# Kernel tuning notes

Measured on AMD Instinct MI355X. Metric: run time of the kernel, lower is better.

Reference implementation:

```python
import jax, jax.numpy as jnp
import numpy as np

B, S, IN_DIM = 2, 2048, 1024
DIMS, QH, KVH = 1024, 16, 4
HD = DIMS // QH          # head_dims = 64
G = QH // KVH            # groups = 4


def setup_inputs() -> dict:
    key = jax.random.key(0)
    k1, k2, k3, k4, k5, k6 = jax.random.split(key, 6)
    scale = 0.02
    q_in = jax.random.normal(k1, (B, S, IN_DIM), dtype=jnp.float32)
    kv_in = jax.random.normal(k2, (B, S, IN_DIM), dtype=jnp.float32)
    # causal mask (True = attend)
    mask = jnp.tril(jnp.ones((S, S), dtype=bool))
    Wq = jax.random.normal(k3, (IN_DIM, QH, HD), dtype=jnp.float32) * scale
    Wk = jax.random.normal(k4, (IN_DIM, KVH, HD), dtype=jnp.float32) * scale
    Wv = jax.random.normal(k5, (IN_DIM, KVH, HD), dtype=jnp.float32) * scale
    Wo = jax.random.normal(k6, (KVH * HD, IN_DIM), dtype=jnp.float32) * scale
    return {"q_in": q_in, "kv_in": kv_in, "mask": mask,
            "Wq": Wq, "Wk": Wk, "Wv": Wv, "Wo": Wo}


def reference(q_in, kv_in, mask, Wq, Wk, Wv, Wo):
    b, s, _ = q_in.shape
    # projections (DenseGeneral, no bias)
    q = jnp.einsum('bsi,ihd->bshd', q_in, Wq)   # [B,S,QH,HD]
    k = jnp.einsum('bsi,ihd->bshd', kv_in, Wk)  # [B,S,KVH,HD]
    v = jnp.einsum('bsi,ihd->bshd', kv_in, Wv)  # [B,S,KVH,HD]
    # rearrange '... s (h g) d -> ... g h s d' with g=G (h outer, g inner),
    # then einsum '... g h s d, ... h a d -> ... h s a' sums over g.
    # Equivalent (and cheaper): sum q over the group axis first.
    q_g = q.reshape(b, s, KVH, G, HD).sum(axis=3)        # [B,S,KVH,HD]
    q_g = jnp.transpose(q_g, (0, 2, 1, 3))               # [B,KVH,S,HD]
    k = jnp.transpose(k, (0, 2, 1, 3))                   # [B,KVH,S,HD]
    v = jnp.transpose(v, (0, 2, 1, 3))                   # [B,KVH,S,HD]
    scores = jnp.einsum('bhsd,bhad->bhsa', q_g, k)       # [B,KVH,S,S]
    scores = jnp.where(mask[None, None, :, :], scores, -jnp.inf)
    attn = jax.nn.softmax(scores / (HD ** 0.5), axis=-1)
    out = jnp.einsum('bhsa,bhad->bhsd', attn, v)         # [B,KVH,S,HD]
    out = jnp.transpose(out, (0, 2, 1, 3)).reshape(b, s, KVH * HD)
    return out @ Wo                                      # [B,S,IN_DIM]
```

## Files before the change

kernel.cpp:

```cpp
#include <hip/hip_runtime.h>
#include <hip/hip_bf16.h>

#define SS 2048
#define NSPLIT 8

typedef __attribute__((ext_vector_type(8))) short bf16x8;
typedef __attribute__((ext_vector_type(4))) float f32x4;

__device__ __forceinline__ short f2bf(float f){
    unsigned u = __float_as_uint(f);
    u += 0x7fff + ((u >> 16) & 1);
    return (short)(u >> 16);
}
__device__ __forceinline__ float bf2f(short s){
    return __uint_as_float(((unsigned)(unsigned short)s) << 16);
}

__global__ __launch_bounds__(256) void k_prep_w(const float* __restrict__ Wq,
                                                const float* __restrict__ Wk,
                                                const float* __restrict__ Wv,
                                                const float* __restrict__ Wo,
                                                short* __restrict__ WcatT,
                                                short* __restrict__ WoT){
    __shared__ float Ts[64][65];
    const int bx = blockIdx.x;
    const int r  = threadIdx.x >> 2;
    const int cq = (threadIdx.x & 3) * 16;
    if (bx < 192) {
        const int ktile = bx & 15, ntile = bx >> 4;
        const int k0 = ktile * 64, n0 = ntile * 64;
        if (ntile < 4) {
            const float* base = Wq + (size_t)(k0 + r) * 1024 + ntile * 256;
            #pragma unroll
            for (int i = 0; i < 16; i += 4) {
                float4 a = *(const float4*)(base + cq + i);
                float4 b = *(const float4*)(base + 64 + cq + i);
                float4 c = *(const float4*)(base + 128 + cq + i);
                float4 d = *(const float4*)(base + 192 + cq + i);
                Ts[r][cq+i]   = 0.125f * (a.x + b.x + c.x + d.x);
                Ts[r][cq+i+1] = 0.125f * (a.y + b.y + c.y + d.y);
                Ts[r][cq+i+2] = 0.125f * (a.z + b.z + c.z + d.z);
                Ts[r][cq+i+3] = 0.125f * (a.w + b.w + c.w + d.w);
            }
        } else {
            const float* W = (ntile < 8) ? Wk : Wv;
            const float* base = W + (size_t)(k0 + r) * 256 + (ntile & 3) * 64;
            #pragma unroll
            for (int i = 0; i < 16; i += 4) {
                float4 a = *(const float4*)(base + cq + i);
                Ts[r][cq+i] = a.x; Ts[r][cq+i+1] = a.y;
                Ts[r][cq+i+2] = a.z; Ts[r][cq+i+3] = a.w;
            }
        }
        __syncthreads();
        short tmp[16];
        #pragma unroll
        for (int i = 0; i < 16; ++i) tmp[i] = f2bf(Ts[cq+i][r]);
        short* dst = WcatT + (size_t)(n0 + r) * 1024 + k0 + cq;
        *(bf16x8*)dst       = *(bf16x8*)&tmp[0];
        *(bf16x8*)(dst + 8) = *(bf16x8*)&tmp[8];
    } else {
        const int b2 = bx - 192;
        const int ktile = b2 & 3, ntile = b2 >> 2;
        const int k0 = ktile * 64, n0 = ntile * 64;
        const float* base = Wo + (size_t)(k0 + r) * 1024 + n0;
        #pragma unroll
        for (int i = 0; i < 16; i += 4) {
            float4 a = *(const float4*)(base + cq + i);
            Ts[r][cq+i] = a.x; Ts[r][cq+i+1] = a.y;
            Ts[r][cq+i+2] = a.z; Ts[r][cq+i+3] = a.w;
        }
        __syncthreads();
        short tmp[16];
        #pragma unroll
        for (int i = 0; i < 16; ++i) tmp[i] = f2bf(Ts[cq+i][r]);
        short* dst = WoT + (size_t)(n0 + r) * 256 + k0 + cq;
        *(bf16x8*)dst       = *(bf16x8*)&tmp[0];
        *(bf16x8*)(dst + 8) = *(bf16x8*)&tmp[8];
    }
}

#define AS(r, c) SMEM[(r) * 72 + (c)]
#define BS(r, c) SMEM[128 * 72 + (r) * 72 + (c)]
__global__ __launch_bounds__(256) void k_gemm1(const float* __restrict__ q_in,
                                               const float* __restrict__ kv_in,
                                               const short* __restrict__ WcatT,
                                               short* __restrict__ pqk,
                                               short* __restrict__ vt){
    const int m0 = blockIdx.x * 128;
    const int n0 = blockIdx.y * 128;
    const float* X = (n0 < 256) ? q_in : kv_in;
    const int tid = threadIdx.x;
    const int wave = tid >> 6, lane = tid & 63, quad = lane >> 4, l16 = lane & 15;
    const int wrow = (wave & 1) * 64, wcol = (wave >> 1) * 64;
    const int r = tid >> 2, cc = (tid & 3) * 16;

    __shared__ short SMEM[2 * 128 * 72];

    f32x4 acc[4][4];
    #pragma unroll
    for (int tm = 0; tm < 4; ++tm)
        #pragma unroll
        for (int tn = 0; tn < 4; ++tn) acc[tm][tn] = f32x4{0.f,0.f,0.f,0.f};

    short ta0[16], ta1[16];
    bf16x8 rb0, rb1, rb2, rb3;
    {
        const float* a0 = X + (size_t)(m0 + r) * 1024 + cc;
        const float* a1 = a0 + (size_t)64 * 1024;
        #pragma unroll
        for (int i = 0; i < 16; i += 4) {
            float4 f = *(const float4*)(a0 + i);
            ta0[i] = f2bf(f.x); ta0[i+1] = f2bf(f.y); ta0[i+2] = f2bf(f.z); ta0[i+3] = f2bf(f.w);
            float4 g = *(const float4*)(a1 + i);
            ta1[i] = f2bf(g.x); ta1[i+1] = f2bf(g.y); ta1[i+2] = f2bf(g.z); ta1[i+3] = f2bf(g.w);
        }
        const short* b0 = WcatT + (size_t)(n0 + r) * 1024 + cc;
        const short* b1 = b0 + (size_t)64 * 1024;
        rb0 = *(const bf16x8*)b0; rb1 = *(const bf16x8*)(b0 + 8);
        rb2 = *(const bf16x8*)b1; rb3 = *(const bf16x8*)(b1 + 8);
    }

    for (int k0 = 0; k0 < 1024; k0 += 64) {
        *(bf16x8*)&AS(r, cc)          = *(bf16x8*)&ta0[0];
        *(bf16x8*)&AS(r, cc + 8)      = *(bf16x8*)&ta0[8];
        *(bf16x8*)&AS(r + 64, cc)     = *(bf16x8*)&ta1[0];
        *(bf16x8*)&AS(r + 64, cc + 8) = *(bf16x8*)&ta1[8];
        *(bf16x8*)&BS(r, cc)          = rb0;
        *(bf16x8*)&BS(r, cc + 8)      = rb1;
        *(bf16x8*)&BS(r + 64, cc)     = rb2;
        *(bf16x8*)&BS(r + 64, cc + 8) = rb3;
        __syncthreads();
        if (k0 + 64 < 1024) {
            const float* a0 = X + (size_t)(m0 + r) * 1024 + k0 + 64 + cc;
            const float* a1 = a0 + (size_t)64 * 1024;
            #pragma unroll
            for (int i = 0; i < 16; i += 4) {
                float4 f = *(const float4*)(a0 + i);
                ta0[i] = f2bf(f.x); ta0[i+1] = f2bf(f.y); ta0[i+2] = f2bf(f.z); ta0[i+3] = f2bf(f.w);
                float4 g = *(const float4*)(a1 + i);
                ta1[i] = f2bf(g.x); ta1[i+1] = f2bf(g.y); ta1[i+2] = f2bf(g.z); ta1[i+3] = f2bf(g.w);
            }
            const short* b0 = WcatT + (size_t)(n0 + r) * 1024 + k0 + 64 + cc;
            const short* b1 = b0 + (size_t)64 * 1024;
            rb0 = *(const bf16x8*)b0; rb1 = *(const bf16x8*)(b0 + 8);
            rb2 = *(const bf16x8*)b1; rb3 = *(const bf16x8*)(b1 + 8);
        }
        #pragma unroll
        for (int ks = 0; ks < 2; ++ks) {
            bf16x8 a[4];
            #pragma unroll
            for (int tm = 0; tm < 4; ++tm)
                a[tm] = *(bf16x8*)&AS(wrow + tm * 16 + l16, ks * 32 + quad * 8);
            #pragma unroll
            for (int tn = 0; tn < 4; ++tn) {
                bf16x8 b = *(bf16x8*)&BS(wcol + tn * 16 + l16, ks * 32 + quad * 8);
                #pragma unroll
                for (int tm = 0; tm < 4; ++tm)
                    acc[tm][tn] = __builtin_amdgcn_mfma_f32_16x16x32_bf16(a[tm], b, acc[tm][tn], 0, 0, 0);
            }
        }
        __syncthreads();
    }
    if (n0 < 512) {
        #pragma unroll
        for (int tm = 0; tm < 4; ++tm) {
            const int mrow = m0 + wrow + tm * 16 + quad * 4;
            #pragma unroll
            for (int tn = 0; tn < 4; ++tn) {
                const int col = n0 + wcol + tn * 16 + l16;
                #pragma unroll
                for (int rg = 0; rg < 4; ++rg)
                    pqk[(size_t)(mrow + rg) * 512 + col] = f2bf(acc[tm][tn][rg]);
            }
        }
    } else {
        #pragma unroll
        for (int tm = 0; tm < 4; ++tm) {
            const int ml = wrow + tm * 16 + quad * 4;
            #pragma unroll
            for (int tn = 0; tn < 4; ++tn) {
                const int cl = wcol + tn * 16 + l16;
                #pragma unroll
                for (int rg = 0; rg < 4; ++rg)
                    SMEM[cl * 136 + ml + rg] = f2bf(acc[tm][tn][rg]);
            }
        }
        __syncthreads();
        const int row  = tid >> 1;
        const int half = tid & 1;
        const int colv = (n0 - 512) + row;
        const int vh = colv >> 6, d = colv & 63;
        const int batch = m0 >> 11;
        const int s0 = (m0 & 2047) + half * 64;
        short* dst = vt + ((size_t)((batch * 4 + vh) * 64 + d)) * 2048 + s0;
        const short* src = &SMEM[row * 136 + half * 64];
        #pragma unroll
        for (int i = 0; i < 64; i += 8)
            *(bf16x8*)(dst + i) = *(const bf16x8*)(src + i);
    }
}

__global__ __launch_bounds__(256) void k_attn4(const short* __restrict__ pqk,
                                               const short* __restrict__ vt,
                                               short* __restrict__ Op,
                                               float* __restrict__ Lp){
    const int bx = blockIdx.x;
    const int qt = 31 - (bx / NSPLIT);
    const int s  = bx - (bx / NSPLIT) * NSPLIT;
    const int kv = blockIdx.y, batch = blockIdx.z;
    const int tid = threadIdx.x;
    const int wave = tid >> 6, lane = tid & 63, quad = lane >> 4, l16 = lane & 15;
    const int r = tid >> 2, c = (tid & 3) * 16;
    const int part = (((batch * 4 + kv) * 32 + qt) * NSPLIT + s);

    __shared__ short Ks[64][72];
    __shared__ short Vs[64][72];
    __shared__ short Ps[64][72];

    const size_t qrow = (size_t)(batch * SS + qt * 64 + wave * 16 + l16);
    bf16x8 aq0 = *(const bf16x8*)(pqk + qrow * 512 + kv * 64 + quad * 8);
    bf16x8 aq1 = *(const bf16x8*)(pqk + qrow * 512 + kv * 64 + 32 + quad * 8);

    f32x4 accO[4];
    #pragma unroll
    for (int t = 0; t < 4; ++t) accO[t] = f32x4{0.f, 0.f, 0.f, 0.f};
    float lrow[4] = {0.f, 0.f, 0.f, 0.f};

    bf16x8 rk0, rk1, rv0, rv1;
    int kt = s;
    if (kt <= qt) {
        const short* ksrc = pqk + (size_t)(batch * SS + kt * 64 + r) * 512 + 256 + kv * 64 + c;
        rk0 = *(const bf16x8*)ksrc; rk1 = *(const bf16x8*)(ksrc + 8);
        const short* vsrc = vt + ((size_t)((batch * 4 + kv) * 64 + r)) * 2048 + kt * 64 + c;
        rv0 = *(const bf16x8*)vsrc; rv1 = *(const bf16x8*)(vsrc + 8);
    }
    for (; kt <= qt; kt += NSPLIT) {
        *(bf16x8*)&Ks[r][c]     = rk0;
        *(bf16x8*)&Ks[r][c + 8] = rk1;
        *(bf16x8*)&Vs[r][c]     = rv0;
        *(bf16x8*)&Vs[r][c + 8] = rv1;
        __syncthreads();
        if (kt + NSPLIT <= qt) {
            const short* ksrc = pqk + (size_t)(batch * SS + (kt + NSPLIT) * 64 + r) * 512 + 256 + kv * 64 + c;
            rk0 = *(const bf16x8*)ksrc; rk1 = *(const bf16x8*)(ksrc + 8);
            const short* vsrc = vt + ((size_t)((batch * 4 + kv) * 64 + r)) * 2048 + (kt + NSPLIT) * 64 + c;
            rv0 = *(const bf16x8*)vsrc; rv1 = *(const bf16x8*)(vsrc + 8);
        }

        f32x4 sc[4];
        #pragma unroll
        for (int t = 0; t < 4; ++t) sc[t] = f32x4{0.f, 0.f, 0.f, 0.f};
        #pragma unroll
        for (int ks = 0; ks < 2; ++ks) {
            bf16x8 a = ks ? aq1 : aq0;
            #pragma unroll
            for (int t = 0; t < 4; ++t) {
                bf16x8 b = *(bf16x8*)&Ks[t * 16 + l16][ks * 32 + quad * 8];
                sc[t] = __builtin_amdgcn_mfma_f32_16x16x32_bf16(a, b, sc[t], 0, 0, 0);
            }
        }
        if (kt == qt) {
            #pragma unroll
            for (int t = 0; t < 4; ++t) {
                int colg = t * 16 + l16;
                #pragma unroll
                for (int rg = 0; rg < 4; ++rg)
                    if (colg > wave * 16 + quad * 4 + rg) sc[t][rg] = -1e30f;
            }
        }
        #pragma unroll
        for (int t = 0; t < 4; ++t) {
            #pragma unroll
            for (int rg = 0; rg < 4; ++rg) {
                float p = __expf(sc[t][rg]);
                lrow[rg] += p;
                Ps[wave * 16 + quad * 4 + rg][t * 16 + l16] = f2bf(p);
            }
        }
        #pragma unroll
        for (int ks = 0; ks < 2; ++ks) {
            bf16x8 ap = *(bf16x8*)&Ps[wave * 16 + l16][ks * 32 + quad * 8];
            #pragma unroll
            for (int t = 0; t < 4; ++t) {
                bf16x8 bv = *(bf16x8*)&Vs[t * 16 + l16][ks * 32 + quad * 8];
                accO[t] = __builtin_amdgcn_mfma_f32_16x16x32_bf16(ap, bv, accO[t], 0, 0, 0);
            }
        }
        __syncthreads();
    }
    #pragma unroll
    for (int rg = 0; rg < 4; ++rg) {
        float l = lrow[rg];
        l += __shfl_xor(l, 1);
        l += __shfl_xor(l, 2);
        l += __shfl_xor(l, 4);
        l += __shfl_xor(l, 8);
        lrow[rg] = l;
    }
    #pragma unroll
    for (int rg = 0; rg < 4; ++rg) {
        int row = wave * 16 + quad * 4 + rg;
        #pragma unroll
        for (int t = 0; t < 4; ++t)
            Op[(size_t)part * 4096 + row * 64 + t * 16 + l16] = f2bf(accO[t][rg]);
    }
    if (l16 == 0) {
        #pragma unroll
        for (int rg = 0; rg < 4; ++rg)
            Lp[part * 64 + (wave * 16 + quad * 4 + rg)] = lrow[rg];
    }
}

__global__ __launch_bounds__(256) void k_combine(const short* __restrict__ Op,
                                                 const float* __restrict__ Lp,
                                                 short* __restrict__ ao){
    const int qt = blockIdx.x, kv = blockIdx.y, batch = blockIdx.z;
    const int tid = threadIdx.x;
    const int rr = tid >> 2, cs = (tid & 3) * 16;
    const int pbase = ((batch * 4 + kv) * 32 + qt) * NSPLIT;
    float lsum = 0.f;
    #pragma unroll
    for (int i = 0; i < NSPLIT; ++i) lsum += Lp[(pbase + i) * 64 + rr];
    float inv = 1.f / lsum;
    float o[16];
    #pragma unroll
    for (int j = 0; j < 16; ++j) o[j] = 0.f;
    #pragma unroll
    for (int i = 0; i < NSPLIT; ++i) {
        const short* src = Op + (size_t)(pbase + i) * 4096 + rr * 64 + cs;
        bf16x8 v0 = *(const bf16x8*)src;
        bf16x8 v1 = *(const bf16x8*)(src + 8);
        #pragma unroll
        for (int j = 0; j < 8; ++j) { o[j] += bf2f(v0[j]); o[j + 8] += bf2f(v1[j]); }
    }
    short* dst = ao + (size_t)(batch * SS + qt * 64 + rr) * 256 + kv * 64 + cs;
    #pragma unroll
    for (int j = 0; j < 16; ++j)
        dst[j] = f2bf(o[j] * inv);
}

__global__ __launch_bounds__(256) void k_gemm2(const short* __restrict__ ao,
                                               const short* __restrict__ WoT,
                                               float* __restrict__ out){
    const int m0 = blockIdx.x * 128;
    const int n0 = blockIdx.y * 128;
    const int tid = threadIdx.x;
    const int wave = tid >> 6, lane = tid & 63, quad = lane >> 4, l16 = lane & 15;
    const int wrow = (wave & 1) * 64, wcol = (wave >> 1) * 64;
    const int r = tid >> 2, cc = (tid & 3) * 16;

    __shared__ short As[128][72];
    __shared__ short Bs[128][72];

    f32x4 acc[4][4];
    #pragma unroll
    for (int tm = 0; tm < 4; ++tm)
        #pragma unroll
        for (int tn = 0; tn < 4; ++tn) acc[tm][tn] = f32x4{0.f,0.f,0.f,0.f};

    bf16x8 ra0, ra1, ra2, ra3, rb0, rb1, rb2, rb3;
    {
        const short* a0 = ao + (size_t)(m0 + r) * 256 + cc;
        const short* a1 = a0 + (size_t)64 * 256;
        const short* b0 = WoT + (size_t)(n0 + r) * 256 + cc;
        const short* b1 = b0 + (size_t)64 * 256;
        ra0 = *(const bf16x8*)a0; ra1 = *(const bf16x8*)(a0 + 8);
        ra2 = *(const bf16x8*)a1; ra3 = *(const bf16x8*)(a1 + 8);
        rb0 = *(const bf16x8*)b0; rb1 = *(const bf16x8*)(b0 + 8);
        rb2 = *(const bf16x8*)b1; rb3 = *(const bf16x8*)(b1 + 8);
    }
    for (int k0 = 0; k0 < 256; k0 += 64) {
        *(bf16x8*)&As[r][cc]          = ra0;
        *(bf16x8*)&As[r][cc + 8]      = ra1;
        *(bf16x8*)&As[r + 64][cc]     = ra2;
        *(bf16x8*)&As[r + 64][cc + 8] = ra3;
        *(bf16x8*)&Bs[r][cc]          = rb0;
        *(bf16x8*)&Bs[r][cc + 8]      = rb1;
        *(bf16x8*)&Bs[r + 64][cc]     = rb2;
        *(bf16x8*)&Bs[r + 64][cc + 8] = rb3;
        __syncthreads();
        if (k0 + 64 < 256) {
            const short* a0 = ao + (size_t)(m0 + r) * 256 + k0 + 64 + cc;
            const short* a1 = a0 + (size_t)64 * 256;
            const short* b0 = WoT + (size_t)(n0 + r) * 256 + k0 + 64 + cc;
            const short* b1 = b0 + (size_t)64 * 256;
            ra0 = *(const bf16x8*)a0; ra1 = *(const bf16x8*)(a0 + 8);
            ra2 = *(const bf16x8*)a1; ra3 = *(const bf16x8*)(a1 + 8);
            rb0 = *(const bf16x8*)b0; rb1 = *(const bf16x8*)(b0 + 8);
            rb2 = *(const bf16x8*)b1; rb3 = *(const bf16x8*)(b1 + 8);
        }
        #pragma unroll
        for (int ks = 0; ks < 2; ++ks) {
            bf16x8 a[4];
            #pragma unroll
            for (int tm = 0; tm < 4; ++tm)
                a[tm] = *(bf16x8*)&As[wrow + tm * 16 + l16][ks * 32 + quad * 8];
            #pragma unroll
            for (int tn = 0; tn < 4; ++tn) {
                bf16x8 b = *(bf16x8*)&Bs[wcol + tn * 16 + l16][ks * 32 + quad * 8];
                #pragma unroll
                for (int tm = 0; tm < 4; ++tm)
                    acc[tm][tn] = __builtin_amdgcn_mfma_f32_16x16x32_bf16(a[tm], b, acc[tm][tn], 0, 0, 0);
            }
        }
        __syncthreads();
    }
    #pragma unroll
    for (int tm = 0; tm < 4; ++tm) {
        const int mrow = m0 + wrow + tm * 16 + quad * 4;
        #pragma unroll
        for (int tn = 0; tn < 4; ++tn) {
            const int col = n0 + wcol + tn * 16 + l16;
            #pragma unroll
            for (int rg = 0; rg < 4; ++rg)
                out[(size_t)(mrow + rg) * 1024 + col] = acc[tm][tn][rg];
        }
    }
}

extern "C" void kernel_launch(void* const* d_in, const int* in_sizes, int n_in,
                              void* d_out, int out_size, void* d_ws, size_t ws_size,
                              hipStream_t stream) {
    const float* q_in  = (const float*)d_in[0];
    const float* kv_in = (const float*)d_in[1];
    int wqi = 3;
    for (int i = 2; i < n_in; ++i)
        if (in_sizes[i] == 1024 * 16 * 64) { wqi = i; break; }
    const float* Wq = (const float*)d_in[wqi];
    const float* Wk = (const float*)d_in[wqi + 1];
    const float* Wv = (const float*)d_in[wqi + 2];
    const float* Wo = (const float*)d_in[wqi + 3];
    float* out = (float*)d_out;

    char* ws = (char*)d_ws;
    short* WcatT = (short*)(ws);
    short* WoT   = (short*)(ws + 1572864);
    short* ao    = (short*)(ws + 2097152);
    short* pqk   = (short*)(ws + 4194304);
    short* vt    = (short*)(ws + 8388608);
    float* Lp    = (float*)(ws + 10485760);
    short* Op    = (short*)(ws + 33554432);

    hipLaunchKernelGGL(k_prep_w,  dim3(256),     dim3(256), 0, stream,
                       Wq, Wk, Wv, Wo, WcatT, WoT);
    hipLaunchKernelGGL(k_gemm1,   dim3(32, 6),   dim3(256), 0, stream,
                       q_in, kv_in, WcatT, pqk, vt);
    hipLaunchKernelGGL(k_attn4,   dim3(32 * NSPLIT, 4, 2), dim3(256), 0, stream,
                       pqk, vt, Op, Lp);
    hipLaunchKernelGGL(k_combine, dim3(32, 4, 2), dim3(256), 0, stream,
                       Op, Lp, ao);
    hipLaunchKernelGGL(k_gemm2,   dim3(32, 8),   dim3(256), 0, stream,
                       ao, WoT, out);
}
```

Measured before the change: 158.6 us.

## Pre-convert activations to bf16 and stage GEMM1 tiles via direct global-to-LDS loads

The prep kernel gets 256 extra blocks that convert q_in and kv_in to bf16 in workspace. GEMM1 then streams A and B tiles with global_load_lds straight into a double-buffered, XOR-swizzled 64KB LDS layout, replacing register staging with per-tile fp32 conversion. The goal is to cut GEMM1 load and convert overhead and overlap the next tile's fetch with the MFMA work. In exchange it adds a full extra read/write pass over the activations and raises LDS use per block, which may lower occupancy.

```diff
diff --git a/kernel.cpp b/kernel.cpp
--- a/kernel.cpp
+++ b/kernel.cpp
@@ -15,15 +15,44 @@
 __device__ __forceinline__ float bf2f(short s){
     return __uint_as_float(((unsigned)(unsigned short)s) << 16);
 }
+__device__ __forceinline__ void gload_lds16(const void* g, void* l){
+    __builtin_amdgcn_global_load_lds((const __attribute__((address_space(1))) void*)g,
+                                     (__attribute__((address_space(3))) void*)l, 16, 0, 0);
+}
 
 __global__ __launch_bounds__(256) void k_prep_w(const float* __restrict__ Wq,
                                                 const float* __restrict__ Wk,
                                                 const float* __restrict__ Wv,
                                                 const float* __restrict__ Wo,
+                                                const float* __restrict__ q_in,
+                                                const float* __restrict__ kv_in,
                                                 short* __restrict__ WcatT,
-                                                short* __restrict__ WoT){
+                                                short* __restrict__ WoT,
+                                                short* __restrict__ Xb){
+    const int bx = blockIdx.x;
+    if (bx >= 256) {
+        const int b2 = bx - 256;
+        const float* src = (b2 < 128) ? q_in : kv_in;
+        short* dst = Xb + ((b2 < 128) ? (size_t)0 : (size_t)4194304);
+        const int tg = (b2 & 127) * 256 + threadIdx.x;
+        #pragma unroll
+        for (int j = 0; j < 8; ++j) {
+            size_t off = (size_t)tg * 16 + (size_t)j * 524288;
+            float4 f0 = *(const float4*)(src + off);
+            float4 f1 = *(const float4*)(src + off + 4);
+            float4 f2 = *(const float4*)(src + off + 8);
+            float4 f3 = *(const float4*)(src + off + 12);
+            short t[16];
+            t[0]=f2bf(f0.x); t[1]=f2bf(f0.y); t[2]=f2bf(f0.z); t[3]=f2bf(f0.w);
+            t[4]=f2bf(f1.x); t[5]=f2bf(f1.y); t[6]=f2bf(f1.z); t[7]=f2bf(f1.w);
+            t[8]=f2bf(f2.x); t[9]=f2bf(f2.y); t[10]=f2bf(f2.z); t[11]=f2bf(f2.w);
+            t[12]=f2bf(f3.x); t[13]=f2bf(f3.y); t[14]=f2bf(f3.z); t[15]=f2bf(f3.w);
+            *(bf16x8*)(dst + off)     = *(bf16x8*)&t[0];
+            *(bf16x8*)(dst + off + 8) = *(bf16x8*)&t[8];
+        }
+        return;
+    }
     __shared__ float Ts[64][65];
-    const int bx = blockIdx.x;
     const int r  = threadIdx.x >> 2;
     const int cq = (threadIdx.x & 3) * 16;
     if (bx < 192) {
@@ -80,22 +109,18 @@
     }
 }
 
-#define AS(r, c) SMEM[(r) * 72 + (c)]
-#define BS(r, c) SMEM[128 * 72 + (r) * 72 + (c)]
-__global__ __launch_bounds__(256) void k_gemm1(const float* __restrict__ q_in,
-                                               const float* __restrict__ kv_in,
+__global__ __launch_bounds__(256) void k_gemm1(const short* __restrict__ Xb,
                                                const short* __restrict__ WcatT,
                                                short* __restrict__ pqk,
                                                short* __restrict__ vt){
     const int m0 = blockIdx.x * 128;
     const int n0 = blockIdx.y * 128;
-    const float* X = (n0 < 256) ? q_in : kv_in;
+    const short* X = Xb + ((n0 < 256) ? (size_t)0 : (size_t)4194304);
     const int tid = threadIdx.x;
     const int wave = tid >> 6, lane = tid & 63, quad = lane >> 4, l16 = lane & 15;
     const int wrow = (wave & 1) * 64, wcol = (wave >> 1) * 64;
-    const int r = tid >> 2, cc = (tid & 3) * 16;
-
-    __shared__ short SMEM[2 * 128 * 72];
+
+    __shared__ char SMEM[65536];
 
     f32x4 acc[4][4];
     #pragma unroll
@@ -103,65 +128,47 @@
         #pragma unroll
         for (int tn = 0; tn < 4; ++tn) acc[tm][tn] = f32x4{0.f,0.f,0.f,0.f};
 
-    short ta0[16], ta1[16];
-    bf16x8 rb0, rb1, rb2, rb3;
-    {
-        const float* a0 = X + (size_t)(m0 + r) * 1024 + cc;
-        const float* a1 = a0 + (size_t)64 * 1024;
-        #pragma unroll
-        for (int i = 0; i < 16; i += 4) {
-            float4 f = *(const float4*)(a0 + i);
-            ta0[i] = f2bf(f.x); ta0[i+1] = f2bf(f.y); ta0[i+2] = f2bf(f.z); ta0[i+3] = f2bf(f.w);
-            float4 g = *(const float4*)(a1 + i);
-            ta1[i] = f2bf(g.x); ta1[i+1] = f2bf(g.y); ta1[i+2] = f2bf(g.z); ta1[i+3] = f2bf(g.w);
-        }
-        const short* b0 = WcatT + (size_t)(n0 + r) * 1024 + cc;
-        const short* b1 = b0 + (size_t)64 * 1024;
-        rb0 = *(const bf16x8*)b0; rb1 = *(const bf16x8*)(b0 + 8);
-        rb2 = *(const bf16x8*)b1; rb3 = *(const bf16x8*)(b1 + 8);
-    }
-
+    const int lr8 = lane >> 3;
+    const int sb  = ((lane & 7) * 16) ^ (lr8 << 4);
+    const char* Abase = (const char*)X     + (size_t)m0 * 2048;
+    const char* Bbase = (const char*)WcatT + (size_t)n0 * 2048;
+
+    auto STAGE = [&](int buf, int k0) {
+        #pragma unroll
+        for (int j = 0; j < 4; ++j) {
+            const int row = wave * 32 + j * 8 + lr8;
+            const size_t goff = (size_t)row * 2048 + (size_t)k0 * 2 + sb;
+            gload_lds16(Abase + goff, SMEM + buf * 32768 + wave * 4096 + j * 1024);
+            gload_lds16(Bbase + goff, SMEM + buf * 32768 + 16384 + wave * 4096 + j * 1024);
+        }
+    };
+
+    STAGE(0, 0);
     for (int k0 = 0; k0 < 1024; k0 += 64) {
-        *(bf16x8*)&AS(r, cc)          = *(bf16x8*)&ta0[0];
-        *(bf16x8*)&AS(r, cc + 8)      = *(bf16x8*)&ta0[8];
-        *(bf16x8*)&AS(r + 64, cc)     = *(bf16x8*)&ta1[0];
-        *(bf16x8*)&AS(r + 64, cc + 8) = *(bf16x8*)&ta1[8];
-        *(bf16x8*)&BS(r, cc)          = rb0;
-        *(bf16x8*)&BS(r, cc + 8)      = rb1;
-        *(bf16x8*)&BS(r + 64, cc)     = rb2;
-        *(bf16x8*)&BS(r + 64, cc + 8) = rb3;
-        __syncthreads();
-        if (k0 + 64 < 1024) {
-            const float* a0 = X + (size_t)(m0 + r) * 1024 + k0 + 64 + cc;
-            const float* a1 = a0 + (size_t)64 * 1024;
-            #pragma unroll
-            for (int i = 0; i < 16; i += 4) {
-                float4 f = *(const float4*)(a0 + i);
-                ta0[i] = f2bf(f.x); ta0[i+1] = f2bf(f.y); ta0[i+2] = f2bf(f.z); ta0[i+3] = f2bf(f.w);
-                float4 g = *(const float4*)(a1 + i);
-                ta1[i] = f2bf(g.x); ta1[i+1] = f2bf(g.y); ta1[i+2] = f2bf(g.z); ta1[i+3] = f2bf(g.w);
-            }
-            const short* b0 = WcatT + (size_t)(n0 + r) * 1024 + k0 + 64 + cc;
-            const short* b1 = b0 + (size_t)64 * 1024;
-            rb0 = *(const bf16x8*)b0; rb1 = *(const bf16x8*)(b0 + 8);
-            rb2 = *(const bf16x8*)b1; rb3 = *(const bf16x8*)(b1 + 8);
-        }
+        __syncthreads();
+        const int cur = (k0 >> 6) & 1;
+        if (k0 + 64 < 1024) STAGE(cur ^ 1, k0 + 64);
         #pragma unroll
         for (int ks = 0; ks < 2; ++ks) {
+            const int cswz = ((ks * 64 + quad * 16) ^ ((l16 & 7) << 4));
             bf16x8 a[4];
             #pragma unroll
-            for (int tm = 0; tm < 4; ++tm)
-                a[tm] = *(bf16x8*)&AS(wrow + tm * 16 + l16, ks * 32 + quad * 8);
+            for (int tm = 0; tm < 4; ++tm) {
+                const int R = wrow + tm * 16 + l16;
+                a[tm] = *(const bf16x8*)(SMEM + cur * 32768 + R * 128 + cswz);
+            }
             #pragma unroll
             for (int tn = 0; tn < 4; ++tn) {
-                bf16x8 b = *(bf16x8*)&BS(wcol + tn * 16 + l16, ks * 32 + quad * 8);
+                const int R2 = wcol + tn * 16 + l16;
+                bf16x8 b = *(const bf16x8*)(SMEM + cur * 32768 + 16384 + R2 * 128 + cswz);
                 #pragma unroll
                 for (int tm = 0; tm < 4; ++tm)
                     acc[tm][tn] = __builtin_amdgcn_mfma_f32_16x16x32_bf16(a[tm], b, acc[tm][tn], 0, 0, 0);
             }
         }
-        __syncthreads();
-    }
+    }
+    __syncthreads();
+
     if (n0 < 512) {
         #pragma unroll
         for (int tm = 0; tm < 4; ++tm) {
@@ -175,6 +182,7 @@
             }
         }
     } else {
+        short* SM16 = (short*)SMEM;
         #pragma unroll
         for (int tm = 0; tm < 4; ++tm) {
             const int ml = wrow + tm * 16 + quad * 4;
@@ -183,7 +191,7 @@
                 const int cl = wcol + tn * 16 + l16;
                 #pragma unroll
                 for (int rg = 0; rg < 4; ++rg)
-                    SMEM[cl * 136 + ml + rg] = f2bf(acc[tm][tn][rg]);
+                    SM16[cl * 136 + ml + rg] = f2bf(acc[tm][tn][rg]);
             }
         }
         __syncthreads();
@@ -194,7 +202,7 @@
         const int batch = m0 >> 11;
         const int s0 = (m0 & 2047) + half * 64;
         short* dst = vt + ((size_t)((batch * 4 + vh) * 64 + d)) * 2048 + s0;
-        const short* src = &SMEM[row * 136 + half * 64];
+        const short* src = &SM16[row * 136 + half * 64];
         #pragma unroll
         for (int i = 0; i < 64; i += 8)
             *(bf16x8*)(dst + i) = *(const bf16x8*)(src + i);
@@ -441,11 +449,12 @@
     short* vt    = (short*)(ws + 8388608);
     float* Lp    = (float*)(ws + 10485760);
     short* Op    = (short*)(ws + 33554432);
-
-    hipLaunchKernelGGL(k_prep_w,  dim3(256),     dim3(256), 0, stream,
-                       Wq, Wk, Wv, Wo, WcatT, WoT);
+    short* Xb    = (short*)(ws + 50331648);
+
+    hipLaunchKernelGGL(k_prep_w,  dim3(512),     dim3(256), 0, stream,
+                       Wq, Wk, Wv, Wo, q_in, kv_in, WcatT, WoT, Xb);
     hipLaunchKernelGGL(k_gemm1,   dim3(32, 6),   dim3(256), 0, stream,
-                       q_in, kv_in, WcatT, pqk, vt);
+                       Xb, WcatT, pqk, vt);
     hipLaunchKernelGGL(k_attn4,   dim3(32 * NSPLIT, 4, 2), dim3(256), 0, stream,
                        pqk, vt, Op, Lp);
     hipLaunchKernelGGL(k_combine, dim3(32, 4, 2), dim3(256), 0, stream,
```

After: 146.6 us. -7.6%, faster.
